# Kernel optimization log

Measured on AMD Instinct MI355X. Metric: run time of the kernel, lower is better.

The kernel has to match this reference:

```python
import jax, jax.numpy as jnp
import numpy as np

FEATURE_DIM = 1024
HIDDEN_DIM = FEATURE_DIM // 4  # MetaNet default: max(input_dim//4, output_dim) = 256
NUM_TASKS = 8
BATCH = 8192


def setup_inputs() -> dict:
    key = jax.random.key(0)
    ks = jax.random.split(key, 8)
    features = jax.random.normal(ks[0], (BATCH, FEATURE_DIM), dtype=jnp.float32)
    # meta_net: Linear(D->H) -> ReLU -> Linear(H->K). Scaled so coefficients straddle the threshold.
    W1 = jax.random.normal(ks[1], (HIDDEN_DIM, FEATURE_DIM), dtype=jnp.float32) * 0.02
    b1 = jax.random.normal(ks[2], (HIDDEN_DIM,), dtype=jnp.float32) * 0.01
    W2 = jax.random.normal(ks[3], (NUM_TASKS, HIDDEN_DIM), dtype=jnp.float32) * 0.1
    b2 = jax.random.normal(ks[4], (NUM_TASKS,), dtype=jnp.float32) * 0.05
    # per-task feature transforms, init randn * 0.01 as in the module
    task_mats = jax.random.normal(ks[5], (NUM_TASKS, FEATURE_DIM, FEATURE_DIM), dtype=jnp.float32) * 0.01
    # projection initialized to identity (nn.init.eye_)
    proj_W = jnp.eye(FEATURE_DIM, dtype=jnp.float32)
    base_threshold = jnp.array([0.05], dtype=jnp.float32)
    beta = jnp.array([1.0], dtype=jnp.float32)
    return {"features": features, "W1": W1, "b1": b1, "W2": W2, "b2": b2,
            "task_mats": task_mats, "proj_W": proj_W,
            "base_threshold": base_threshold, "beta": beta}


def reference(features, W1, b1, W2, b2, task_mats, proj_W, base_threshold, beta):
    # --- meta_net forward: coefficients [B, K] ---
    h = features @ W1.T + b1                    # [B, H]
    relu_h = jnp.maximum(h, 0.0)
    coeffs = relu_h @ W2.T + b2                 # [B, K]

    # --- gradient-based uncertainty: ||d coeff_k / d features_b||_2 ---
    # Jacobian of the 2-layer MLP: J[b,k,d] = sum_h W2[k,h] * relu'(h[b,h]) * W1[h,d]
    mask = (h > 0).astype(features.dtype)       # [B, H]
    J = jnp.einsum('kh,bh,hd->bkd', W2, mask, W1)   # [B, K, D]
    unc = jnp.sqrt(jnp.sum(J * J, axis=-1))     # [B, K]
    mx = jnp.max(unc)
    unc = jnp.where(mx > 0, unc / mx, unc)
    # torch computes this on detached features with create_graph=False -> non-differentiable
    unc = jax.lax.stop_gradient(unc)

    # --- adaptive gating ---
    base = jax.nn.softplus(base_threshold)                  # [1]
    thresholds = base * (1.0 + jax.nn.relu(beta) * unc)     # [B, K]
    gated = jnp.where(jnp.abs(coeffs) < thresholds, 0.0, coeffs)  # [B, K]

    # --- sequential weighted task-vector combination (blockwise=False) ---
    x = features                                # [B, D]
    for j in range(task_mats.shape[0]):         # small fixed K, structurally sequential
        x = x + gated[:, j:j + 1] * (x @ task_mats[j])
    return x @ proj_W.T                         # [B, D]
```

## Files before the change

kernel.cpp:

```cpp
#include <hip/hip_runtime.h>


typedef float  f32x4  __attribute__((ext_vector_type(4)));
typedef __bf16 bf16x8 __attribute__((ext_vector_type(8)));
typedef _Float16 f16x8 __attribute__((ext_vector_type(8)));
typedef _Float16 f16x4 __attribute__((ext_vector_type(4)));

__device__ __forceinline__ unsigned short f2bf(float x) {
  return __builtin_bit_cast(unsigned short, (__bf16)x);
}
__device__ __forceinline__ float bf2f(unsigned short u) {
  return (float)__builtin_bit_cast(__bf16, u);
}
__device__ __forceinline__ void ldsload16(void* lds, const void* g) {
  __builtin_amdgcn_global_load_lds(
      (const __attribute__((address_space(1))) void*)g,
      (__attribute__((address_space(3))) void*)lds, 16, 0, 0);
}


__global__ __launch_bounds__(256) void k_initsplit2(const float* __restrict__ F,
                                                    float* __restrict__ xout,
                                                    unsigned short* __restrict__ xhA,
                                                    unsigned short* __restrict__ xhB) {
  size_t i = (size_t)blockIdx.x * 256 + threadIdx.x;
  float4 f = *(const float4*)&F[i * 4];
  *(float4*)&xout[i * 4] = f;
  ushort4 u;
  u.x = f2bf(f.x); u.y = f2bf(f.y); u.z = f2bf(f.z); u.w = f2bf(f.w);
  *(ushort4*)&xhA[i * 4] = u;
  *(ushort4*)&xhB[i * 4] = u;
}

__global__ __launch_bounds__(256) void k_prep1(const float* __restrict__ W1,
                                               _Float16* __restrict__ hi,
                                               _Float16* __restrict__ lo,
                                               float* __restrict__ G) {
  __shared__ float Wa[16][33], Wb[16][33];
  int t = threadIdx.x;
  if (blockIdx.x < 256) {
    size_t i = (size_t)blockIdx.x * 256 + t;
    float4 f = *(const float4*)&W1[i * 4];
    _Float16 h0 = (_Float16)f.x, h1 = (_Float16)f.y, h2 = (_Float16)f.z, h3 = (_Float16)f.w;
    *(f16x4*)&hi[i * 4] = (f16x4){h0, h1, h2, h3};
    *(f16x4*)&lo[i * 4] = (f16x4){(_Float16)((f.x - (float)h0) * 2048.0f),
                                  (_Float16)((f.y - (float)h1) * 2048.0f),
                                  (_Float16)((f.z - (float)h2) * 2048.0f),
                                  (_Float16)((f.w - (float)h3) * 2048.0f)};
    return;
  }
  int bid2 = blockIdx.x - 256;
  int bi = bid2 & 15, bj = bid2 >> 4;
  int ti = t & 15, tj = t >> 4;
  float acc = 0.f;
  for (int kc = 0; kc < 1024; kc += 32) {
    __syncthreads();
    for (int e = t; e < 512; e += 256) {
      int r = e >> 5, k = e & 31;
      Wa[r][k] = W1[(size_t)(bi * 16 + r) * 1024 + kc + k];
      Wb[r][k] = W1[(size_t)(bj * 16 + r) * 1024 + kc + k];
    }
    __syncthreads();
#pragma unroll
    for (int k = 0; k < 32; k++) acc += Wa[ti][k] * Wb[tj][k];
  }
  G[(size_t)(bi * 16 + ti) * 256 + bj * 16 + tj] = acc;
}

__global__ __launch_bounds__(256) void k_prepA(const float* __restrict__ W2,
                                               const float* __restrict__ G,
                                               unsigned short* __restrict__ Bk,
                                               unsigned int* __restrict__ mx,
                                               int* __restrict__ cnt,
                                               int* __restrict__ cnt2,
                                               unsigned int* __restrict__ flag) {
  int k = blockIdx.x >> 8, hr = blockIdx.x & 255, t = threadIdx.x;
  if (blockIdx.x == 0) {
    if (t == 0) { *mx = 0u; *flag = 1u; }
    if (t < 8) { cnt[t] = 0; cnt2[t] = 0; }
  }
  float v = W2[k * 256 + hr] * W2[k * 256 + t] * G[(size_t)hr * 256 + t];
  float hi = bf2f(f2bf(v));
  float lo = v - hi;
  unsigned short* row = &Bk[((size_t)k * 256 + hr) * 512];
  row[t] = f2bf(hi);
  row[256 + t] = f2bf(lo);
}

__global__ __launch_bounds__(256) void k_maskcoef(const float* __restrict__ h,
                                                  const float* __restrict__ W2,
                                                  const float* __restrict__ b2,
                                                  unsigned short* __restrict__ Mb,
                                                  unsigned int* __restrict__ Mbits,
                                                  float* __restrict__ coeffs) {
  __shared__ float W2s[2048];
  __shared__ unsigned sw[4][8];
  int t = threadIdx.x;
  for (int e = t; e < 2048; e += 256) W2s[e] = W2[e];
  int w = t >> 6, l = t & 63;
  int row = blockIdx.x * 4 + w;
  float4 hv = *(const float4*)&h[(size_t)row * 256 + l * 4];
  ushort4 mv;
  mv.x = hv.x > 0.f ? 0x3F80 : 0; mv.y = hv.y > 0.f ? 0x3F80 : 0;
  mv.z = hv.z > 0.f ? 0x3F80 : 0; mv.w = hv.w > 0.f ? 0x3F80 : 0;
  *(ushort4*)&Mb[(size_t)row * 256 + l * 4] = mv;
  unsigned nib = (hv.x > 0.f ? 1u : 0u) | (hv.y > 0.f ? 2u : 0u) |
                 (hv.z > 0.f ? 4u : 0u) | (hv.w > 0.f ? 8u : 0u);
  if (l < 8) sw[w][l] = 0u;
  __syncthreads();
  atomicOr(&sw[w][l >> 3], nib << ((l & 7) * 4));
  __syncthreads();
  if (l < 8) Mbits[row * 8 + l] = sw[w][l];
  float r0 = fmaxf(hv.x, 0.f), r1 = fmaxf(hv.y, 0.f);
  float r2 = fmaxf(hv.z, 0.f), r3 = fmaxf(hv.w, 0.f);
#pragma unroll
  for (int k = 0; k < 8; k++) {
    const float* wr = &W2s[k * 256 + l * 4];
    float p = r0 * wr[0] + r1 * wr[1] + r2 * wr[2] + r3 * wr[3];
    p += __shfl_xor(p, 1);  p += __shfl_xor(p, 2);  p += __shfl_xor(p, 4);
    p += __shfl_xor(p, 8);  p += __shfl_xor(p, 16); p += __shfl_xor(p, 32);
    if (l == 0) coeffs[row * 8 + k] = p + b2[k];
  }
}

__global__ __launch_bounds__(256) void k_gateidx(const float* __restrict__ coeffs,
                                                 const float* __restrict__ unc2,
                                                 const unsigned int* __restrict__ mxb,
                                                 const float* __restrict__ btp,
                                                 const float* __restrict__ betap,
                                                 unsigned short* __restrict__ rowidx,
                                                 float* __restrict__ gcomp,
                                                 int* __restrict__ cnt,
                                                 unsigned short* __restrict__ rowidx2,
                                                 int* __restrict__ cnt2) {
  __shared__ int lc[8], base[8], lc2[8], base2[8];
  __shared__ float sgv[256];
  int t = threadIdx.x;
  if (t < 8) { lc[t] = 0; lc2[t] = 0; }
  __syncthreads();
  int i = blockIdx.x * 256 + t;
  float c = coeffs[i];
  float u2 = fmaxf(unc2[i], 0.f);
  float un = sqrtf(u2);
  float m = sqrtf(__uint_as_float(*mxb));
  float u = (m > 0.f) ? un / m : un;
  float base_t = (float)log1p(exp((double)btp[0]));
  float br = fmaxf(betap[0], 0.f);
  float thr = base_t * (1.0f + br * u);
  float gv = (fabsf(c) < thr) ? 0.f : c;
  sgv[t] = gv;
  int jj = i & 7, row = i >> 3, slot = -1;
  if (gv != 0.f) slot = atomicAdd(&lc[jj], 1);
  __syncthreads();
  int slot2 = -1;
  if (jj >= 1 && gv == 0.f && sgv[t - 1] != 0.f) slot2 = atomicAdd(&lc2[jj], 1);
  __syncthreads();
  if (t < 8) {
    base[t]  = lc[t]  ? atomicAdd(&cnt[t],  lc[t])  : 0;
    base2[t] = lc2[t] ? atomicAdd(&cnt2[t], lc2[t]) : 0;
  }
  __syncthreads();
  if (slot >= 0) {
    int pos = base[jj] + slot;
    rowidx[jj * 8192 + pos] = (unsigned short)row;
    gcomp[jj * 8192 + pos] = gv;
  }
  if (slot2 >= 0)
    rowidx2[jj * 8192 + base2[jj] + slot2] = (unsigned short)row;
}

__global__ __launch_bounds__(256) void k_prepTP(const float* __restrict__ TM,
                                                unsigned short* __restrict__ Tb,
                                                const float* __restrict__ P,
                                                unsigned short* __restrict__ Pb,
                                                unsigned int* __restrict__ flag) {
  __shared__ float Ls[64][65];
  int bid = blockIdx.x;
  int t = threadIdx.x;
  if (bid >= 2048) {
    size_t i = (size_t)(bid - 2048) * 256 + t;
    float4 f = *(const float4*)&P[i * 4];
    ushort4 u;
    u.x = f2bf(f.x); u.y = f2bf(f.y); u.z = f2bf(f.z); u.w = f2bf(f.w);
    *(ushort4*)&Pb[i * 4] = u;
    size_t e = i * 4;
    bool bad = false;
#pragma unroll
    for (int s = 0; s < 4; s++) {
      size_t ee = e + s;
      float exp = ((ee >> 10) == (ee & 1023)) ? 1.0f : 0.0f;
      float got = (s == 0) ? f.x : (s == 1) ? f.y : (s == 2) ? f.z : f.w;
      if (got != exp) bad = true;
    }
    if (bad) atomicAnd(flag, 0u);
    return;
  }
  int jj = bid >> 8, kt = (bid >> 4) & 15, nt = bid & 15;
  int r = t >> 2, c0 = (t & 3) * 16;
  const float* src = TM + (size_t)jj * 1048576 + (size_t)(kt * 64 + r) * 1024 + nt * 64 + c0;
  float4 v0 = *(const float4*)&src[0];
  float4 v1 = *(const float4*)&src[4];
  float4 v2 = *(const float4*)&src[8];
  float4 v3 = *(const float4*)&src[12];
  float tmp[16] = {v0.x, v0.y, v0.z, v0.w, v1.x, v1.y, v1.z, v1.w,
                   v2.x, v2.y, v2.z, v2.w, v3.x, v3.y, v3.z, v3.w};
#pragma unroll
  for (int i = 0; i < 16; i++) Ls[r][c0 + i] = tmp[i];
  __syncthreads();
  int nr = t >> 2, kc = (t & 3) * 16;
  union { unsigned short s[16]; uint4 v[2]; } p;
#pragma unroll
  for (int i = 0; i < 16; i++) p.s[i] = f2bf(Ls[kc + i][nr]);
  unsigned short* dst = Tb + (size_t)jj * 1048576 + (size_t)(nt * 64 + nr) * 1024 + kt * 64 + kc;
  *(uint4*)&dst[0] = p.v[0];
  *(uint4*)&dst[8] = p.v[1];
}


__global__ __launch_bounds__(256) void k_gemm_h3(const float* __restrict__ F,
                                                 const _Float16* __restrict__ W1h,
                                                 const _Float16* __restrict__ W1l,
                                                 const float* __restrict__ b1,
                                                 float* __restrict__ hout) {
  __shared__ __attribute__((aligned(16))) float    Af[64 * 32];
  __shared__ __attribute__((aligned(16))) _Float16 Bh[64 * 32];
  __shared__ __attribute__((aligned(16))) _Float16 Bl[64 * 32];
  int t = threadIdx.x, w = t >> 6, l = t & 63, q = l >> 4, li = l & 15;
  int wm = w >> 1, wn = w & 1;
  int ib = blockIdx.x, jb = blockIdx.y;
  f32x4 acc0[2][2] = {}, acc1[2][2] = {};
  int brow = t >> 2, bg = (((t & 3) - (brow >> 1)) & 3) * 8;
  for (int k0 = 0; k0 < 1024; k0 += 32) {
    __syncthreads();
#pragma unroll
    for (int i = 0; i < 2; i++) {
      int slot = i * 256 + t, r = slot >> 3, c = slot & 7;
      int g = c ^ (r & 7);
      ldsload16((void*)(Af + (size_t)(i * 256 + w * 64) * 4),
                F + (size_t)(ib * 64 + r) * 1024 + k0 + g * 4);
    }
    {
      size_t bo = (size_t)(jb * 64 + brow) * 1024 + k0 + bg;
      ldsload16((void*)(Bh + (w * 64) * 8), W1h + bo);
      ldsload16((void*)(Bl + (w * 64) * 8), W1l + bo);
    }
    __syncthreads();
    f16x8 ah[2], al[2], bh[2], bl[2];
#pragma unroll
    for (int mt = 0; mt < 2; mt++) {
      int r = wm * 32 + mt * 16 + li;
      f32x4 a0 = *(const f32x4*)&Af[r * 32 + ((2 * q) ^ (r & 7)) * 4];
      f32x4 a1 = *(const f32x4*)&Af[r * 32 + ((2 * q + 1) ^ (r & 7)) * 4];
#pragma unroll
      for (int jx = 0; jx < 4; jx++) {
        _Float16 h0 = (_Float16)a0[jx];
        ah[mt][jx] = h0;
        al[mt][jx] = (_Float16)((a0[jx] - (float)h0) * 2048.0f);
        _Float16 h1 = (_Float16)a1[jx];
        ah[mt][4 + jx] = h1;
        al[mt][4 + jx] = (_Float16)((a1[jx] - (float)h1) * 2048.0f);
      }
    }
#pragma unroll
    for (int nt = 0; nt < 2; nt++) {
      int rr = wn * 32 + nt * 16 + li;
      int c = ((q + (rr >> 1)) & 3) * 8;
      bh[nt] = *(const f16x8*)&Bh[rr * 32 + c];
      bl[nt] = *(const f16x8*)&Bl[rr * 32 + c];
    }
#pragma unroll
    for (int mt = 0; mt < 2; mt++)
#pragma unroll
      for (int nt = 0; nt < 2; nt++) {
        acc0[mt][nt] = __builtin_amdgcn_mfma_f32_16x16x32_f16(ah[mt], bh[nt], acc0[mt][nt], 0, 0, 0);
        acc1[mt][nt] = __builtin_amdgcn_mfma_f32_16x16x32_f16(ah[mt], bl[nt], acc1[mt][nt], 0, 0, 0);
        acc1[mt][nt] = __builtin_amdgcn_mfma_f32_16x16x32_f16(al[mt], bh[nt], acc1[mt][nt], 0, 0, 0);
      }
  }
  const float sc = 1.0f / 2048.0f;
#pragma unroll
  for (int mt = 0; mt < 2; mt++) {
    int grow = ib * 64 + wm * 32 + mt * 16 + q * 4;
#pragma unroll
    for (int nt = 0; nt < 2; nt++) {
      int gcol = jb * 64 + wn * 32 + nt * 16 + li;
      float bb = b1[gcol];
#pragma unroll
      for (int r = 0; r < 4; r++)
        hout[(size_t)(grow + r) * 256 + gcol] = acc0[mt][nt][r] + acc1[mt][nt][r] * sc + bb;
    }
  }
}

__global__ __launch_bounds__(512) void k_gemm_unc2(const unsigned short* __restrict__ Mb,
                                                   const unsigned short* __restrict__ BkAll,
                                                   const unsigned int* __restrict__ Mbits,
                                                   float* __restrict__ unc2,
                                                   unsigned int* __restrict__ mx) {
  __shared__ __attribute__((aligned(16))) unsigned short As[128 * 32];
  __shared__ __attribute__((aligned(16))) unsigned short Bs[256 * 32];
  __shared__ float Red[128][4];
  int t = threadIdx.x, w = t >> 6, l = t & 63, q = l >> 4, li = l & 15;
  int wm = w >> 2, wn = w & 3;
  int rb = blockIdx.x, kidx = blockIdx.y;
  const unsigned short* Bk = BkAll + (size_t)kidx * 256 * 512;
  f32x4 acc[4][4] = {};
  for (int k0 = 0; k0 < 512; k0 += 32) {
    __syncthreads();
    {
      int row = t >> 2, g = (((t & 3) - (row >> 1)) & 3) * 8;
      ldsload16((void*)(As + (size_t)(w * 64) * 8),
                Mb + (size_t)(rb * 128 + row) * 256 + (k0 & 255) + g);
    }
#pragma unroll
    for (int i = 0; i < 2; i++) {
      int idx = i * 512 + t, row = idx >> 2, g = (((idx & 3) - (row >> 1)) & 3) * 8;
      ldsload16((void*)(Bs + (size_t)(i * 512 + w * 64) * 8),
                Bk + (size_t)row * 512 + k0 + g);
    }
    __syncthreads();
    bf16x8 av[4], bv[4];
#pragma unroll
    for (int mt = 0; mt < 4; mt++) {
      int r = wm * 64 + mt * 16 + li;
      av[mt] = *(const bf16x8*)&As[r * 32 + ((q + (r >> 1)) & 3) * 8];
    }
#pragma unroll
    for (int nt = 0; nt < 4; nt++) {
      int rc = wn * 64 + nt * 16 + li;
      bv[nt] = *(const bf16x8*)&Bs[rc * 32 + ((q + (rc >> 1)) & 3) * 8];
    }
#pragma unroll
    for (int mt = 0; mt < 4; mt++)
#pragma unroll
      for (int nt = 0; nt < 4; nt++)
        acc[mt][nt] = __builtin_amdgcn_mfma_f32_16x16x32_bf16(av[mt], bv[nt], acc[mt][nt], 0, 0, 0);
  }
#pragma unroll
  for (int mt = 0; mt < 4; mt++) {
#pragma unroll
    for (int r = 0; r < 4; r++) {
      int rl = wm * 64 + mt * 16 + q * 4 + r;
      int grow = rb * 128 + rl;
      unsigned m0 = Mbits[(size_t)grow * 8 + wn * 2];
      unsigned m1 = Mbits[(size_t)grow * 8 + wn * 2 + 1];
      float p = 0.f;
#pragma unroll
      for (int nt = 0; nt < 4; nt++) {
        unsigned mword = (nt < 2) ? m0 : m1;
        int sh = (nt & 1) * 16 + li;
        if ((mword >> sh) & 1u) p += acc[mt][nt][r];
      }
      p += __shfl_xor(p, 1); p += __shfl_xor(p, 2);
      p += __shfl_xor(p, 4); p += __shfl_xor(p, 8);
      if (li == 0) Red[rl][wn] = p;
    }
  }
  __syncthreads();
  if (t < 128) {
    float s = Red[t][0] + Red[t][1] + Red[t][2] + Red[t][3];
    unc2[(size_t)(rb * 128 + t) * 8 + kidx] = s;
    float v = fmaxf(s, 0.f);
#pragma unroll
    for (int d = 1; d < 64; d <<= 1) v = fmaxf(v, __shfl_xor(v, d));
    if ((t & 63) == 0) atomicMax(mx, __float_as_uint(v));
  }
}

__global__ __launch_bounds__(1024) void k_chain8(const unsigned short* __restrict__ cur,
                                                 unsigned short* __restrict__ nxt,
                                                 const unsigned short* __restrict__ Tb,
                                                 const unsigned short* __restrict__ rowidx,
                                                 const int* __restrict__ cnt,
                                                 const unsigned short* __restrict__ rowidx2,
                                                 const int* __restrict__ cnt2,
                                                 const float* __restrict__ gcomp,
                                                 float* __restrict__ xout, int j) {
  int Mj = min(max(cnt[j], 0), 8192);
  __shared__ __attribute__((aligned(16))) unsigned short As[64 * 512];
  __shared__ __attribute__((aligned(16))) unsigned short Bs[64 * 512];
  int t = threadIdx.x, w = t >> 6, l = t & 63, q = l >> 4, li = l & 15;
  int wm = w >> 2, wn = w & 3;
  int bx = blockIdx.x, jb = blockIdx.y;
  int bid = jb * 16 + bx;
  const unsigned short* ridx = rowidx + j * 8192;
  {
    int M2 = min(max(cnt2[j], 0), 8192);
    for (int cm2 = bid; cm2 < M2; cm2 += 256) {
      int row = rowidx2[j * 8192 + cm2] & 8191;
      if (t < 128)
        *(uint4*)&nxt[(size_t)row * 1024 + t * 8] =
            *(const uint4*)&cur[(size_t)row * 1024 + t * 8];
    }
  }
  for (int ib = bx; ib * 64 < Mj; ib += 16) {
    f32x4 acc = {};
#pragma unroll 1
    for (int half = 0; half < 2; half++) {
      __syncthreads();
#pragma unroll
      for (int i = 0; i < 4; i++) {
        int slot = i * 1024 + t;
        int r = slot >> 6, kcs = slot & 63;
        int kcg = kcs ^ (r & 7);
        int cm = ib * 64 + r;
        int grow = ridx[cm < Mj ? cm : Mj - 1] & 8191;
        ldsload16((void*)(As + (size_t)(i * 1024 + w * 64) * 8),
                  cur + (size_t)grow * 1024 + half * 512 + kcg * 8);
      }
#pragma unroll
      for (int i = 0; i < 4; i++) {
        int slot = i * 1024 + t;
        int n = slot >> 6, kcs = slot & 63;
        int kcg = kcs ^ (n & 7);
        ldsload16((void*)(Bs + (size_t)(i * 1024 + w * 64) * 8),
                  Tb + (size_t)(jb * 64 + n) * 1024 + half * 512 + kcg * 8);
      }
      __syncthreads();
#pragma unroll
      for (int s = 0; s < 16; s++) {
        int r = wm * 16 + li;
        bf16x8 av = *(const bf16x8*)&As[((size_t)r * 64 + ((s * 4 + q) ^ (r & 7))) * 8];
        int n = wn * 16 + li;
        bf16x8 bv = *(const bf16x8*)&Bs[((size_t)n * 64 + ((s * 4 + q) ^ (n & 7))) * 8];
        acc = __builtin_amdgcn_mfma_f32_16x16x32_bf16(av, bv, acc, 0, 0, 0);
      }
    }
#pragma unroll
    for (int r = 0; r < 4; r++) {
      int cm = ib * 64 + wm * 16 + q * 4 + r;
      if (cm >= Mj) continue;
      int grow = ridx[cm] & 8191;
      float g = gcomp[j * 8192 + cm];
      size_t off = (size_t)grow * 1024 + jb * 64 + wn * 16 + li;
      float xv = fmaf(g, acc[r], xout[off]);
      xout[off] = xv;
      nxt[off] = f2bf(xv);
    }
  }
}

__global__ __launch_bounds__(256) void k_proj3(const unsigned short* __restrict__ xcur,
                                               const unsigned short* __restrict__ Pb,
                                               float* __restrict__ out,
                                               const unsigned int* __restrict__ flag) {
  if (*flag) return;
  __shared__ __attribute__((aligned(16))) unsigned short As[128 * 32];
  __shared__ __attribute__((aligned(16))) unsigned short Bs[128 * 32];
  int t = threadIdx.x, w = t >> 6, l = t & 63, q = l >> 4, li = l & 15;
  int wm = w >> 1, wn = w & 1;
  int ib = blockIdx.x, jb = blockIdx.y;
  f32x4 acc[4][4] = {};
  for (int k0 = 0; k0 < 1024; k0 += 32) {
    __syncthreads();
    const unsigned short* ga = xcur + (size_t)(ib * 128) * 1024 + k0;
    const unsigned short* gb = Pb + (size_t)(jb * 128) * 1024 + k0;
#pragma unroll
    for (int i = 0; i < 2; i++) {
      int idx = i * 256 + t, row = idx >> 2, kc = (idx & 3) * 8;
      ldsload16((void*)(As + (i * 256 + w * 64) * 8), ga + (size_t)row * 1024 + kc);
      ldsload16((void*)(Bs + (i * 256 + w * 64) * 8), gb + (size_t)row * 1024 + kc);
    }
    __syncthreads();
    bf16x8 av[4], bv[4];
#pragma unroll
    for (int mt = 0; mt < 4; mt++)
      av[mt] = *(const bf16x8*)&As[(wm * 64 + mt * 16 + li) * 32 + q * 8];
#pragma unroll
    for (int nt = 0; nt < 4; nt++)
      bv[nt] = *(const bf16x8*)&Bs[(wn * 64 + nt * 16 + li) * 32 + q * 8];
#pragma unroll
    for (int mt = 0; mt < 4; mt++)
#pragma unroll
      for (int nt = 0; nt < 4; nt++)
        acc[mt][nt] = __builtin_amdgcn_mfma_f32_16x16x32_bf16(av[mt], bv[nt], acc[mt][nt], 0, 0, 0);
  }
#pragma unroll
  for (int mt = 0; mt < 4; mt++) {
    int grow = ib * 128 + wm * 64 + mt * 16 + q * 4;
#pragma unroll
    for (int nt = 0; nt < 4; nt++) {
      int gcol = jb * 128 + wn * 64 + nt * 16 + li;
#pragma unroll
      for (int r = 0; r < 4; r++)
        out[(size_t)(grow + r) * 1024 + gcol] = acc[mt][nt][r];
    }
  }
}


extern "C" void kernel_launch(void* const* d_in, const int* in_sizes, int n_in,
                              void* d_out, int out_size, void* d_ws, size_t ws_size,
                              hipStream_t stream) {
  const float* F    = (const float*)d_in[0];
  const float* W1   = (const float*)d_in[1];
  const float* b1   = (const float*)d_in[2];
  const float* W2   = (const float*)d_in[3];
  const float* b2   = (const float*)d_in[4];
  const float* TM   = (const float*)d_in[5];
  const float* PW   = (const float*)d_in[6];
  const float* bt   = (const float*)d_in[7];
  const float* beta = (const float*)d_in[8];

  char* w = (char*)d_ws;
  float*          hbuf   = (float*)         (w + 0);
  unsigned short* Mb     = (unsigned short*)(w + 8388608);
  unsigned int*   Mbits  = (unsigned int*)  (w + 12582912);
  float*          coeffs = (float*)         (w + 12845056);
  float*          unc2   = (float*)         (w + 13107200);
  float*          G      = (float*)         (w + 13369344);
  unsigned short* Bk     = (unsigned short*)(w + 13631488);
  _Float16*       W1h    = (_Float16*)      (w + 15728640);
  _Float16*       W1l    = (_Float16*)      (w + 16252928);
  unsigned short* Tb     = (unsigned short*)(w + 0);
  char*           buf1   =                  (w + 33554432);
  unsigned int*   mx     = (unsigned int*)  (w + 50331648);
  int*            cnt    = (int*)           (w + 50331652);
  int*            cnt2   = (int*)           (w + 50331684);
  unsigned int*   flag   = (unsigned int*)  (w + 50331716);
  unsigned short* rowidx = (unsigned short*)(w + 50332160);
  unsigned short* rowidx2= (unsigned short*)(w + 50463232);
  float*          gcomp  = (float*)         (w + 50594304);
  unsigned short* xhA    = (unsigned short*)(w + 50856448);
  unsigned short* xhB    = (unsigned short*)(w + 67633664);
  float* xout = (float*)d_out;

  k_initsplit2<<<8192, 256, 0, stream>>>(F, xout, xhA, xhB);
  k_prep1<<<512, 256, 0, stream>>>(W1, W1h, W1l, G);
  k_gemm_h3<<<dim3(128, 4), 256, 0, stream>>>(F, W1h, W1l, b1, hbuf);
  k_maskcoef<<<2048, 256, 0, stream>>>(hbuf, W2, b2, Mb, Mbits, coeffs);
  k_prepA<<<2048, 256, 0, stream>>>(W2, G, Bk, mx, cnt, cnt2, flag);
  k_gemm_unc2<<<dim3(64, 8), 512, 0, stream>>>(Mb, Bk, Mbits, unc2, mx);
  k_gateidx<<<256, 256, 0, stream>>>(coeffs, unc2, mx, bt, beta,
                                     rowidx, gcomp, cnt, rowidx2, cnt2);

  unsigned short* Pb = (unsigned short*)buf1;
  k_prepTP<<<3072, 256, 0, stream>>>(TM, Tb, PW, Pb, flag);
  for (int j = 0; j < 8; j++) {
    const unsigned short* cur = (j & 1) ? xhB : xhA;
    unsigned short*       nxt = (j & 1) ? xhA : xhB;
    k_chain8<<<dim3(16, 16), 1024, 0, stream>>>(cur, nxt, Tb + (size_t)j * 1048576,
                                                rowidx, cnt, rowidx2, cnt2,
                                                gcomp, xout, j);
  }

  k_proj3<<<dim3(64, 8), 256, 0, stream>>>(xhA, Pb, xout, flag);
}
```

Before: 354.4 us.

## Restructure chain GEMM into split-K warps with larger register tiles

```diff
diff --git a/kernel.cpp b/kernel.cpp
--- a/kernel.cpp
+++ b/kernel.cpp
@@ -367,7 +367,7 @@
   }
 }
 
-__global__ __launch_bounds__(1024) void k_chain8(const unsigned short* __restrict__ cur,
+__global__ __launch_bounds__(512) void k_chain10(const unsigned short* __restrict__ cur,
                                                  unsigned short* __restrict__ nxt,
                                                  const unsigned short* __restrict__ Tb,
                                                  const unsigned short* __restrict__ rowidx,
@@ -377,65 +377,101 @@
                                                  const float* __restrict__ gcomp,
                                                  float* __restrict__ xout, int j) {
   int Mj = min(max(cnt[j], 0), 8192);
-  __shared__ __attribute__((aligned(16))) unsigned short As[64 * 512];
-  __shared__ __attribute__((aligned(16))) unsigned short Bs[64 * 512];
+  __shared__ __attribute__((aligned(16))) unsigned short smem[128 * 512];
+  unsigned short* As = smem;
+  unsigned short* Bs = smem + 64 * 512;
+  float* planes = (float*)smem;
   int t = threadIdx.x, w = t >> 6, l = t & 63, q = l >> 4, li = l & 15;
-  int wm = w >> 2, wn = w & 3;
+  int kq = w >> 1;
+  int nh = w & 1;
   int bx = blockIdx.x, jb = blockIdx.y;
   int bid = jb * 16 + bx;
   const unsigned short* ridx = rowidx + j * 8192;
   {
     int M2 = min(max(cnt2[j], 0), 8192);
-    for (int cm2 = bid; cm2 < M2; cm2 += 256) {
+    int sub = t >> 7, tc = t & 127;
+    for (int cm2 = bid * 4 + sub; cm2 < M2; cm2 += 1024) {
       int row = rowidx2[j * 8192 + cm2] & 8191;
-      if (t < 128)
-        *(uint4*)&nxt[(size_t)row * 1024 + t * 8] =
-            *(const uint4*)&cur[(size_t)row * 1024 + t * 8];
+      *(uint4*)&nxt[(size_t)row * 1024 + tc * 8] =
+          *(const uint4*)&cur[(size_t)row * 1024 + tc * 8];
     }
   }
   for (int ib = bx; ib * 64 < Mj; ib += 16) {
-    f32x4 acc = {};
+    f32x4 acc[4][2] = {};
 #pragma unroll 1
     for (int half = 0; half < 2; half++) {
       __syncthreads();
 #pragma unroll
-      for (int i = 0; i < 4; i++) {
-        int slot = i * 1024 + t;
+      for (int i = 0; i < 8; i++) {
+        int slot = i * 512 + t;
         int r = slot >> 6, kcs = slot & 63;
         int kcg = kcs ^ (r & 7);
         int cm = ib * 64 + r;
         int grow = ridx[cm < Mj ? cm : Mj - 1] & 8191;
-        ldsload16((void*)(As + (size_t)(i * 1024 + w * 64) * 8),
+        ldsload16((void*)(As + (size_t)(i * 512 + w * 64) * 8),
                   cur + (size_t)grow * 1024 + half * 512 + kcg * 8);
       }
 #pragma unroll
-      for (int i = 0; i < 4; i++) {
-        int slot = i * 1024 + t;
+      for (int i = 0; i < 8; i++) {
+        int slot = i * 512 + t;
         int n = slot >> 6, kcs = slot & 63;
         int kcg = kcs ^ (n & 7);
-        ldsload16((void*)(Bs + (size_t)(i * 1024 + w * 64) * 8),
+        ldsload16((void*)(Bs + (size_t)(i * 512 + w * 64) * 8),
                   Tb + (size_t)(jb * 64 + n) * 1024 + half * 512 + kcg * 8);
       }
       __syncthreads();
-#pragma unroll
-      for (int s = 0; s < 16; s++) {
-        int r = wm * 16 + li;
-        bf16x8 av = *(const bf16x8*)&As[((size_t)r * 64 + ((s * 4 + q) ^ (r & 7))) * 8];
-        int n = wn * 16 + li;
-        bf16x8 bv = *(const bf16x8*)&Bs[((size_t)n * 64 + ((s * 4 + q) ^ (n & 7))) * 8];
-        acc = __builtin_amdgcn_mfma_f32_16x16x32_bf16(av, bv, acc, 0, 0, 0);
-      }
-    }
-#pragma unroll
-    for (int r = 0; r < 4; r++) {
-      int cm = ib * 64 + wm * 16 + q * 4 + r;
-      if (cm >= Mj) continue;
-      int grow = ridx[cm] & 8191;
-      float g = gcomp[j * 8192 + cm];
-      size_t off = (size_t)grow * 1024 + jb * 64 + wn * 16 + li;
-      float xv = fmaf(g, acc[r], xout[off]);
-      xout[off] = xv;
-      nxt[off] = f2bf(xv);
+      if ((kq >> 1) == half) {
+        int sbase = (kq & 1) * 8;
+#pragma unroll
+        for (int sl = 0; sl < 8; sl++) {
+          int s = sbase + sl;
+          bf16x8 av[4], bv[2];
+#pragma unroll
+          for (int mt = 0; mt < 4; mt++) {
+            int r = mt * 16 + li;
+            av[mt] = *(const bf16x8*)&As[((size_t)r * 64 + ((s * 4 + q) ^ (r & 7))) * 8];
+          }
+#pragma unroll
+          for (int ntl = 0; ntl < 2; ntl++) {
+            int n = (nh * 2 + ntl) * 16 + li;
+            bv[ntl] = *(const bf16x8*)&Bs[((size_t)n * 64 + ((s * 4 + q) ^ (n & 7))) * 8];
+          }
+#pragma unroll
+          for (int mt = 0; mt < 4; mt++)
+#pragma unroll
+            for (int ntl = 0; ntl < 2; ntl++)
+              acc[mt][ntl] = __builtin_amdgcn_mfma_f32_16x16x32_bf16(av[mt], bv[ntl], acc[mt][ntl], 0, 0, 0);
+        }
+      }
+    }
+    __syncthreads();
+    {
+      float* pw = planes + kq * 4352;
+#pragma unroll
+      for (int mt = 0; mt < 4; mt++)
+#pragma unroll
+        for (int ntl = 0; ntl < 2; ntl++)
+#pragma unroll
+          for (int r = 0; r < 4; r++)
+            pw[(mt * 16 + q * 4 + r) * 68 + nh * 32 + ntl * 16 + li] = acc[mt][ntl][r];
+    }
+    __syncthreads();
+    {
+      int c = t & 63, r0 = (t >> 6) * 8;
+#pragma unroll
+      for (int i = 0; i < 8; i++) {
+        int r = r0 + i;
+        int cm = ib * 64 + r;
+        if (cm >= Mj) continue;
+        int grow = ridx[cm] & 8191;
+        float g = gcomp[j * 8192 + cm];
+        float s = planes[0 * 4352 + r * 68 + c] + planes[1 * 4352 + r * 68 + c] +
+                  planes[2 * 4352 + r * 68 + c] + planes[3 * 4352 + r * 68 + c];
+        size_t off = (size_t)grow * 1024 + jb * 64 + c;
+        float xv = fmaf(g, s, xout[off]);
+        xout[off] = xv;
+        nxt[off] = f2bf(xv);
+      }
     }
   }
 }
@@ -539,7 +575,7 @@
   for (int j = 0; j < 8; j++) {
     const unsigned short* cur = (j & 1) ? xhB : xhA;
     unsigned short*       nxt = (j & 1) ? xhA : xhB;
-    k_chain8<<<dim3(16, 16), 1024, 0, stream>>>(cur, nxt, Tb + (size_t)j * 1048576,
+    k_chain10<<<dim3(16, 16), 512, 0, stream>>>(cur, nxt, Tb + (size_t)j * 1048576,
                                                 rowidx, cnt, rowidx2, cnt2,
                                                 gcomp, xout, j);
   }
```

After: 359.8 us. No clear change (+1.5%).
